# Optimization experiments

Hardware: AMD Instinct MI355X
Metric: run time of the kernel (lower is better)

Reference implementation:

```python
import jax, jax.numpy as jnp
import numpy as np

# The 16 differentiable binary logic gates used by difflogic are all of the form
# c0 + c1*a + c2*b + c3*(a*b). Rows are gate ids 0..15.
GATE_COEF = jnp.array([
    [0., 0., 0., 0.],    # 0: False
    [0., 0., 0., 1.],    # 1: a AND b
    [0., 1., 0., -1.],   # 2: a AND NOT b
    [0., 1., 0., 0.],    # 3: a
    [0., 0., 1., -1.],   # 4: NOT a AND b
    [0., 0., 1., 0.],    # 5: b
    [0., 1., 1., -2.],   # 6: XOR
    [0., 1., 1., -1.],   # 7: OR
    [1., -1., -1., 1.],  # 8: NOR
    [1., -1., -1., 2.],  # 9: XNOR
    [1., 0., -1., 0.],   # 10: NOT b
    [1., 0., -1., 1.],   # 11: a OR NOT b (b implies a)
    [1., -1., 0., 0.],   # 12: NOT a
    [1., -1., 0., 1.],   # 13: NOT a OR b (a implies b)
    [1., 0., 0., -1.],   # 14: NAND
    [1., 0., 0., 0.],    # 15: True
], dtype=jnp.float32)

BATCH = 256
IN_DIM = 1024
WIDTH = 64000
K = 10
TAU = 30.0


def _logic_layer(x, w, idx_a, idx_b):
    # x: [B, in_dim], w: [out, 16], idx_*: [out] int32
    a = x[:, idx_a]            # [B, out]
    b = x[:, idx_b]            # [B, out]
    coef = jax.nn.softmax(w, axis=-1) @ GATE_COEF   # [out, 4]
    return coef[:, 0] + coef[:, 1] * a + coef[:, 2] * b + coef[:, 3] * (a * b)


def setup_inputs() -> dict:
    key = jax.random.key(0)
    ks = jax.random.split(key, 10)
    x = jax.random.uniform(ks[0], (BATCH, IN_DIM), dtype=jnp.float32)
    w1 = jax.random.normal(ks[1], (WIDTH, 16), dtype=jnp.float32)
    w2 = jax.random.normal(ks[2], (WIDTH, 16), dtype=jnp.float32)
    w3 = jax.random.normal(ks[3], (WIDTH, 16), dtype=jnp.float32)
    idx_a1 = jax.random.randint(ks[4], (WIDTH,), 0, IN_DIM, dtype=jnp.int32)
    idx_b1 = jax.random.randint(ks[5], (WIDTH,), 0, IN_DIM, dtype=jnp.int32)
    idx_a2 = jax.random.randint(ks[6], (WIDTH,), 0, WIDTH, dtype=jnp.int32)
    idx_b2 = jax.random.randint(ks[7], (WIDTH,), 0, WIDTH, dtype=jnp.int32)
    idx_a3 = jax.random.randint(ks[8], (WIDTH,), 0, WIDTH, dtype=jnp.int32)
    idx_b3 = jax.random.randint(ks[9], (WIDTH,), 0, WIDTH, dtype=jnp.int32)
    return {"x": x, "w1": w1, "w2": w2, "w3": w3,
            "idx_a1": idx_a1, "idx_b1": idx_b1,
            "idx_a2": idx_a2, "idx_b2": idx_b2,
            "idx_a3": idx_a3, "idx_b3": idx_b3}


def reference(x, w1, w2, w3, idx_a1, idx_b1, idx_a2, idx_b2, idx_a3, idx_b3):
    h = _logic_layer(x, w1, idx_a1, idx_b1)
    h = _logic_layer(h, w2, idx_a2, idx_b2)
    h = _logic_layer(h, w3, idx_a3, idx_b3)
    # GroupSum: [B, WIDTH] -> [B, K, WIDTH//K] -> sum -> / tau
    return h.reshape(h.shape[0], K, -1).sum(axis=-1) / TAU
```

## Files before the change

kernel.cpp:

```cpp
#include <hip/hip_runtime.h>
#include <hip/hip_bf16.h>
#include <stdint.h>


#define BATCH   256
#define IN_DIM  1024
#define WIDTH   64000
#define NGROUP  10
#define GSIZE   6400
#define TAU     30.0f
#define NWAVE   16
#define GPW     8
#define GPB     (NWAVE*GPW)
#define NBLK    (WIDTH/GPB)

typedef unsigned short ushort_t;

static __device__ __forceinline__ float bf2f(ushort_t s) {
    return __uint_as_float((uint32_t)s << 16);
}
static __device__ __forceinline__ ushort_t f2bf(float f) {
    uint32_t u = __float_as_uint(f);
    return (ushort_t)((u + 0x7fffu + ((u >> 16) & 1u)) >> 16);
}

__global__ __launch_bounds__(256) void transpose_kernel(
    const float* __restrict__ x, ushort_t* __restrict__ xT)
{
    __shared__ float tile[64][65];
    const int c0 = (blockIdx.x & 15) * 64;
    const int b0 = (blockIdx.x >> 4) * 64;
    const int lt = threadIdx.x & 63;
    const int wt = threadIdx.x >> 6;
    for (int r = wt; r < 64; r += 4)
        tile[r][lt] = x[(b0 + r) * IN_DIM + c0 + lt];
    __syncthreads();
    for (int r = wt; r < 64; r += 4)
        xT[(c0 + r) * BATCH + b0 + lt] = f2bf(tile[lt][r]);
}

__global__ __launch_bounds__(256) void coef_kernel(
    const float* __restrict__ w1, const float* __restrict__ w2,
    const float* __restrict__ w3,
    float4* __restrict__ c1o, float4* __restrict__ c2o, float4* __restrict__ c3o)
{
    const int id = blockIdx.x * 256 + threadIdx.x;
    const int layer = id / WIDTH;
    const int j = id - layer * WIDTH;
    const float* w = (layer == 0) ? w1 : (layer == 1) ? w2 : w3;
    float4* cc     = (layer == 0) ? c1o : (layer == 1) ? c2o : c3o;

    const float4* w4 = (const float4*)(w + (size_t)j * 16);
    float4 q0 = w4[0], q1 = w4[1], q2 = w4[2], q3 = w4[3];
    float p[16] = {q0.x,q0.y,q0.z,q0.w, q1.x,q1.y,q1.z,q1.w,
                   q2.x,q2.y,q2.z,q2.w, q3.x,q3.y,q3.z,q3.w};
    float m = p[0];
    #pragma unroll
    for (int i = 1; i < 16; ++i) m = fmaxf(m, p[i]);
    float s = 0.f;
    #pragma unroll
    for (int i = 0; i < 16; ++i) { p[i] = __expf(p[i] - m); s += p[i]; }
    const float inv = 1.0f / s;

    float c0 = (p[8]+p[9]+p[10]+p[11]+p[12]+p[13]+p[14]+p[15]) * inv;
    float c1 = (p[2]+p[3]+p[6]+p[7] - p[8]-p[9]-p[12]-p[13]) * inv;
    float c2 = (p[4]+p[5]+p[6]+p[7] - p[8]-p[9]-p[10]-p[11]) * inv;
    float c3 = (p[1]-p[2]-p[4]-2.f*p[6]-p[7]+p[8]+2.f*p[9]+p[11]+p[13]-p[14]) * inv;
    cc[j] = make_float4(c0, c1, c2, c3);
}

template<bool FINAL>
__global__ __launch_bounds__(1024) void logic_layer_kernel(
    const ushort_t* __restrict__ in,
    const float4*   __restrict__ coefs,
    const int*      __restrict__ ia,
    const int*      __restrict__ ib,
    ushort_t*       __restrict__ out,
    float*          __restrict__ red_out)
{
    const int lane = threadIdx.x & 63;
    const int wave = __builtin_amdgcn_readfirstlane(threadIdx.x >> 6);
    const int jw = blockIdx.x * GPB + wave * GPW;

    int av[GPW], bv[GPW];
    #pragma unroll
    for (int u = 0; u < GPW; ++u) { av[u] = ia[jw + u]; bv[u] = ib[jw + u]; }

    float4 acc = make_float4(0.f, 0.f, 0.f, 0.f);

    #pragma unroll
    for (int u = 0; u < GPW; ++u) {
        const float4 c = coefs[jw + u];
        const ushort4 a4 = ((const ushort4*)(in + (size_t)av[u] * BATCH))[lane];
        const ushort4 b4 = ((const ushort4*)(in + (size_t)bv[u] * BATCH))[lane];
        const float Ax = bf2f(a4.x), Ay = bf2f(a4.y), Az = bf2f(a4.z), Aw = bf2f(a4.w);
        const float Bx = bf2f(b4.x), By = bf2f(b4.y), Bz = bf2f(b4.z), Bw = bf2f(b4.w);
        float4 r;
        r.x = fmaf(c.w, Ax * Bx, fmaf(c.z, Bx, fmaf(c.y, Ax, c.x)));
        r.y = fmaf(c.w, Ay * By, fmaf(c.z, By, fmaf(c.y, Ay, c.x)));
        r.z = fmaf(c.w, Az * Bz, fmaf(c.z, Bz, fmaf(c.y, Az, c.x)));
        r.w = fmaf(c.w, Aw * Bw, fmaf(c.z, Bw, fmaf(c.y, Aw, c.x)));
        if (FINAL) {
            acc.x += r.x; acc.y += r.y; acc.z += r.z; acc.w += r.w;
        } else {
            ushort4 o;
            o.x = f2bf(r.x); o.y = f2bf(r.y); o.z = f2bf(r.z); o.w = f2bf(r.w);
            ((ushort4*)(out + (size_t)(jw + u) * BATCH))[lane] = o;
        }
    }

    if (FINAL) {
        __shared__ float4 s[NWAVE][64];
        s[wave][lane] = acc;
        __syncthreads();
        if (wave == 0) {
            float4 t = s[0][lane];
            #pragma unroll
            for (int w = 1; w < NWAVE; ++w) {
                float4 q = s[w][lane];
                t.x += q.x; t.y += q.y; t.z += q.z; t.w += q.w;
            }
            const float sc = 1.0f / TAU;
            const int grp = (blockIdx.x * GPB) / GSIZE;
            const int b0 = lane * 4;
            atomicAdd(&red_out[(b0 + 0) * NGROUP + grp], t.x * sc);
            atomicAdd(&red_out[(b0 + 1) * NGROUP + grp], t.y * sc);
            atomicAdd(&red_out[(b0 + 2) * NGROUP + grp], t.z * sc);
            atomicAdd(&red_out[(b0 + 3) * NGROUP + grp], t.w * sc);
        }
    }
}

extern "C" void kernel_launch(void* const* d_in, const int* in_sizes, int n_in,
                              void* d_out, int out_size, void* d_ws, size_t ws_size,
                              hipStream_t stream)
{
    const float* x   = (const float*)d_in[0];
    const float* w1  = (const float*)d_in[1];
    const float* w2  = (const float*)d_in[2];
    const float* w3  = (const float*)d_in[3];
    const int*   ia1 = (const int*)d_in[4];
    const int*   ib1 = (const int*)d_in[5];
    const int*   ia2 = (const int*)d_in[6];
    const int*   ib2 = (const int*)d_in[7];
    const int*   ia3 = (const int*)d_in[8];
    const int*   ib3 = (const int*)d_in[9];
    float* out = (float*)d_out;

    char* ws = (char*)d_ws;
    ushort_t* xT = (ushort_t*)ws;
    ushort_t* h1 = (ushort_t*)(ws + ((size_t)IN_DIM * BATCH * 2));
    ushort_t* h2 = h1 + (size_t)WIDTH * BATCH;
    float*    c1 = (float*)(h2 + (size_t)WIDTH * BATCH);
    float*    c2 = c1 + (size_t)WIDTH * 4;
    float*    c3 = c2 + (size_t)WIDTH * 4;

    hipMemsetAsync(d_out, 0, (size_t)out_size * sizeof(float), stream);

    transpose_kernel<<<64, 256, 0, stream>>>(x, xT);
    coef_kernel<<<(3 * WIDTH) / 256, 256, 0, stream>>>(w1, w2, w3,
                                                       (float4*)c1, (float4*)c2, (float4*)c3);

    logic_layer_kernel<false><<<NBLK, 1024, 0, stream>>>(
        xT, (const float4*)c1, ia1, ib1, h1, nullptr);
    logic_layer_kernel<false><<<NBLK, 1024, 0, stream>>>(
        h1, (const float4*)c2, ia2, ib2, h2, nullptr);
    logic_layer_kernel<true><<<NBLK, 1024, 0, stream>>>(
        h2, (const float4*)c3, ia3, ib3, nullptr, out);
}
```

Measured before the change: 141.7 us.

## Fuse three logic layers by composing index trees into per-output leaf gathers

Precomputes, for each final-layer output, the eight leaf input indices and seven gate coefficient sets through the index chains of layers 2 and 3. One fused kernel then evaluates the whole depth-3 tree per output straight from the transposed bf16 input and reduces into the group sums. This removes the writes and scattered reads of the two 64000x256 intermediate activations and two kernel launches. In exchange, shared first- and second-layer nodes are recomputed per output, giving roughly twice the gate arithmetic and eight gathers per output, all from the small 512KB input. Intermediates now stay in fp32 instead of being rounded to bf16.

```diff
diff --git a/kernel.cpp b/kernel.cpp
--- a/kernel.cpp
+++ b/kernel.cpp
@@ -1,5 +1,4 @@
 #include <hip/hip_runtime.h>
-#include <hip/hip_bf16.h>
 #include <stdint.h>
 
 
@@ -22,6 +21,17 @@
 static __device__ __forceinline__ ushort_t f2bf(float f) {
     uint32_t u = __float_as_uint(f);
     return (ushort_t)((u + 0x7fffu + ((u >> 16) & 1u)) >> 16);
+}
+static __device__ __forceinline__ float4 up4(ushort4 s) {
+    return make_float4(bf2f(s.x), bf2f(s.y), bf2f(s.z), bf2f(s.w));
+}
+static __device__ __forceinline__ float4 gate4(float4 c, float4 a, float4 b) {
+    float4 r;
+    r.x = fmaf(c.w, a.x * b.x, fmaf(c.z, b.x, fmaf(c.y, a.x, c.x)));
+    r.y = fmaf(c.w, a.y * b.y, fmaf(c.z, b.y, fmaf(c.y, a.y, c.x)));
+    r.z = fmaf(c.w, a.z * b.z, fmaf(c.z, b.z, fmaf(c.y, a.z, c.x)));
+    r.w = fmaf(c.w, a.w * b.w, fmaf(c.z, b.w, fmaf(c.y, a.w, c.x)));
+    return r;
 }
 
 __global__ __launch_bounds__(256) void transpose_kernel(
@@ -69,65 +79,99 @@
     cc[j] = make_float4(c0, c1, c2, c3);
 }
 
-template<bool FINAL>
-__global__ __launch_bounds__(1024) void logic_layer_kernel(
-    const ushort_t* __restrict__ in,
-    const float4*   __restrict__ coefs,
-    const int*      __restrict__ ia,
-    const int*      __restrict__ ib,
-    ushort_t*       __restrict__ out,
+__global__ __launch_bounds__(256) void prep_kernel(
+    const int* __restrict__ ia1, const int* __restrict__ ib1,
+    const int* __restrict__ ia2, const int* __restrict__ ib2,
+    const int* __restrict__ ia3, const int* __restrict__ ib3,
+    const float4* __restrict__ c1, const float4* __restrict__ c2,
+    const float4* __restrict__ c3,
+    int* __restrict__ leaf,
+    float4* __restrict__ pc)
+{
+    const int j = blockIdx.x * 256 + threadIdx.x;
+    if (j >= WIDTH) return;
+
+    const int pa = ia3[j], pb = ib3[j];
+    const int qaa = ia2[pa], qab = ib2[pa];
+    const int qba = ia2[pb], qbb = ib2[pb];
+
+    int* L = leaf + (size_t)j * 8;
+    L[0] = ia1[qaa]; L[1] = ib1[qaa];
+    L[2] = ia1[qab]; L[3] = ib1[qab];
+    L[4] = ia1[qba]; L[5] = ib1[qba];
+    L[6] = ia1[qbb]; L[7] = ib1[qbb];
+
+    float4* P = pc + (size_t)j * 7;
+    P[0] = c1[qaa]; P[1] = c1[qab]; P[2] = c1[qba]; P[3] = c1[qbb];
+    P[4] = c2[pa];  P[5] = c2[pb];
+    P[6] = c3[j];
+}
+
+__global__ __launch_bounds__(1024) void fused_kernel(
+    const ushort_t* __restrict__ xT,
+    const int*      __restrict__ leaf,
+    const float4*   __restrict__ pc,
     float*          __restrict__ red_out)
 {
     const int lane = threadIdx.x & 63;
     const int wave = __builtin_amdgcn_readfirstlane(threadIdx.x >> 6);
     const int jw = blockIdx.x * GPB + wave * GPW;
 
-    int av[GPW], bv[GPW];
-    #pragma unroll
-    for (int u = 0; u < GPW; ++u) { av[u] = ia[jw + u]; bv[u] = ib[jw + u]; }
-
     float4 acc = make_float4(0.f, 0.f, 0.f, 0.f);
 
-    #pragma unroll
+    #pragma unroll 2
     for (int u = 0; u < GPW; ++u) {
-        const float4 c = coefs[jw + u];
-        const ushort4 a4 = ((const ushort4*)(in + (size_t)av[u] * BATCH))[lane];
-        const ushort4 b4 = ((const ushort4*)(in + (size_t)bv[u] * BATCH))[lane];
-        const float Ax = bf2f(a4.x), Ay = bf2f(a4.y), Az = bf2f(a4.z), Aw = bf2f(a4.w);
-        const float Bx = bf2f(b4.x), By = bf2f(b4.y), Bz = bf2f(b4.z), Bw = bf2f(b4.w);
-        float4 r;
-        r.x = fmaf(c.w, Ax * Bx, fmaf(c.z, Bx, fmaf(c.y, Ax, c.x)));
-        r.y = fmaf(c.w, Ay * By, fmaf(c.z, By, fmaf(c.y, Ay, c.x)));
-        r.z = fmaf(c.w, Az * Bz, fmaf(c.z, Bz, fmaf(c.y, Az, c.x)));
-        r.w = fmaf(c.w, Aw * Bw, fmaf(c.z, Bw, fmaf(c.y, Aw, c.x)));
-        if (FINAL) {
-            acc.x += r.x; acc.y += r.y; acc.z += r.z; acc.w += r.w;
-        } else {
-            ushort4 o;
-            o.x = f2bf(r.x); o.y = f2bf(r.y); o.z = f2bf(r.z); o.w = f2bf(r.w);
-            ((ushort4*)(out + (size_t)(jw + u) * BATCH))[lane] = o;
+        const int j = jw + u;
+        const int* Lp = leaf + (size_t)j * 8;
+        const int l0 = __builtin_amdgcn_readfirstlane(Lp[0]);
+        const int l1 = __builtin_amdgcn_readfirstlane(Lp[1]);
+        const int l2 = __builtin_amdgcn_readfirstlane(Lp[2]);
+        const int l3 = __builtin_amdgcn_readfirstlane(Lp[3]);
+        const int l4 = __builtin_amdgcn_readfirstlane(Lp[4]);
+        const int l5 = __builtin_amdgcn_readfirstlane(Lp[5]);
+        const int l6 = __builtin_amdgcn_readfirstlane(Lp[6]);
+        const int l7 = __builtin_amdgcn_readfirstlane(Lp[7]);
+
+        const ushort4 v0 = ((const ushort4*)(xT + (size_t)l0 * BATCH))[lane];
+        const ushort4 v1 = ((const ushort4*)(xT + (size_t)l1 * BATCH))[lane];
+        const ushort4 v2 = ((const ushort4*)(xT + (size_t)l2 * BATCH))[lane];
+        const ushort4 v3 = ((const ushort4*)(xT + (size_t)l3 * BATCH))[lane];
+        const ushort4 v4 = ((const ushort4*)(xT + (size_t)l4 * BATCH))[lane];
+        const ushort4 v5 = ((const ushort4*)(xT + (size_t)l5 * BATCH))[lane];
+        const ushort4 v6 = ((const ushort4*)(xT + (size_t)l6 * BATCH))[lane];
+        const ushort4 v7 = ((const ushort4*)(xT + (size_t)l7 * BATCH))[lane];
+
+        const float4* Pp = pc + (size_t)j * 7;
+        const float4 C1aa = Pp[0], C1ab = Pp[1], C1ba = Pp[2], C1bb = Pp[3];
+        const float4 C2a  = Pp[4], C2b  = Pp[5], C3c = Pp[6];
+
+        const float4 haa = gate4(C1aa, up4(v0), up4(v1));
+        const float4 hab = gate4(C1ab, up4(v2), up4(v3));
+        const float4 hba = gate4(C1ba, up4(v4), up4(v5));
+        const float4 hbb = gate4(C1bb, up4(v6), up4(v7));
+        const float4 h2a = gate4(C2a, haa, hab);
+        const float4 h2b = gate4(C2b, hba, hbb);
+        const float4 h3  = gate4(C3c, h2a, h2b);
+        acc.x += h3.x; acc.y += h3.y; acc.z += h3.z; acc.w += h3.w;
+    }
+
+    __shared__ float4 s[NWAVE][64];
+    s[wave][lane] = acc;
+    __syncthreads();
+    if (wave == 0) {
+        float4 t = s[0][lane];
+        #pragma unroll
+        for (int w = 1; w < NWAVE; ++w) {
+            float4 q = s[w][lane];
+            t.x += q.x; t.y += q.y; t.z += q.z; t.w += q.w;
         }
-    }
-
-    if (FINAL) {
-        __shared__ float4 s[NWAVE][64];
-        s[wave][lane] = acc;
-        __syncthreads();
-        if (wave == 0) {
-            float4 t = s[0][lane];
-            #pragma unroll
-            for (int w = 1; w < NWAVE; ++w) {
-                float4 q = s[w][lane];
-                t.x += q.x; t.y += q.y; t.z += q.z; t.w += q.w;
-            }
-            const float sc = 1.0f / TAU;
-            const int grp = (blockIdx.x * GPB) / GSIZE;
-            const int b0 = lane * 4;
-            atomicAdd(&red_out[(b0 + 0) * NGROUP + grp], t.x * sc);
-            atomicAdd(&red_out[(b0 + 1) * NGROUP + grp], t.y * sc);
-            atomicAdd(&red_out[(b0 + 2) * NGROUP + grp], t.z * sc);
-            atomicAdd(&red_out[(b0 + 3) * NGROUP + grp], t.w * sc);
-        }
+        const float sc = 1.0f / TAU;
+        const int grp = (blockIdx.x * GPB) / GSIZE;
+        const int b0 = lane * 4;
+        atomicAdd(&red_out[(b0 + 0) * NGROUP + grp], t.x * sc);
+        atomicAdd(&red_out[(b0 + 1) * NGROUP + grp], t.y * sc);
+        atomicAdd(&red_out[(b0 + 2) * NGROUP + grp], t.z * sc);
+        atomicAdd(&red_out[(b0 + 3) * NGROUP + grp], t.w * sc);
     }
 }
 
@@ -149,22 +193,19 @@
 
     char* ws = (char*)d_ws;
     ushort_t* xT = (ushort_t*)ws;
-    ushort_t* h1 = (ushort_t*)(ws + ((size_t)IN_DIM * BATCH * 2));
-    ushort_t* h2 = h1 + (size_t)WIDTH * BATCH;
-    float*    c1 = (float*)(h2 + (size_t)WIDTH * BATCH);
+    float*    c1 = (float*)(ws + (size_t)IN_DIM * BATCH * 2);
     float*    c2 = c1 + (size_t)WIDTH * 4;
     float*    c3 = c2 + (size_t)WIDTH * 4;
+    int*    leaf = (int*)(c3 + (size_t)WIDTH * 4);
+    float4*   pc = (float4*)(leaf + (size_t)WIDTH * 8);
 
     hipMemsetAsync(d_out, 0, (size_t)out_size * sizeof(float), stream);
 
     transpose_kernel<<<64, 256, 0, stream>>>(x, xT);
     coef_kernel<<<(3 * WIDTH) / 256, 256, 0, stream>>>(w1, w2, w3,
                                                        (float4*)c1, (float4*)c2, (float4*)c3);
-
-    logic_layer_kernel<false><<<NBLK, 1024, 0, stream>>>(
-        xT, (const float4*)c1, ia1, ib1, h1, nullptr);
-    logic_layer_kernel<false><<<NBLK, 1024, 0, stream>>>(
-        h1, (const float4*)c2, ia2, ib2, h2, nullptr);
-    logic_layer_kernel<true><<<NBLK, 1024, 0, stream>>>(
-        h2, (const float4*)c3, ia3, ib3, nullptr, out);
-}
+    prep_kernel<<<WIDTH / 256, 256, 0, stream>>>(ia1, ib1, ia2, ib2, ia3, ib3,
+                                                 (const float4*)c1, (const float4*)c2,
+                                                 (const float4*)c3, leaf, pc);
+    fused_kernel<<<NBLK, 1024, 0, stream>>>(xT, leaf, pc, out);
+}
```

New measurement: 135.0 us. -4.7%, faster.
